# Performance work log

Hardware: AMD Instinct MI355X
Metric: run time of the kernel (lower is better)

The kernel has to match this reference:

```python
import jax, jax.numpy as jnp
import numpy as np

U, I, D, OUT = 8192, 16384, 64, 64

def setup_inputs() -> dict:
    key = jax.random.key(0)
    k1, k2, k3, k4 = jax.random.split(key, 4)
    user_emb = jax.random.normal(k1, (U, D), dtype=jnp.float32)
    item_emb = jax.random.normal(k2, (I, D), dtype=jnp.float32)
    attention_weight = jax.random.normal(k3, (D, OUT), dtype=jnp.float32) * (1.0 / np.sqrt(D))
    adj_matrix = jax.random.randint(k4, (U, I), 0, 2, dtype=jnp.int32)
    return {"user_emb": user_emb, "item_emb": item_emb,
            "attention_weight": attention_weight, "adj_matrix": adj_matrix}

def reference(user_emb, item_emb, attention_weight, adj_matrix):
    # score[u,i] = <user_emb[u], item_emb[i]>  (torch.inner)
    score = jnp.einsum('ud,id->ui', user_emb, item_emb)
    # mask non-edges to 0 (NOT -inf, faithful to torch.where(adj>0, score, 0))
    score = jnp.where(adj_matrix > 0, score, 0.0)
    score = jax.nn.softmax(score, axis=1)
    # flag == True path: aggregate items into users, then project
    output = score @ item_emb          # [U, D]
    output = output @ attention_weight  # [U, OUT]
    return output
```

## Files before the change

### kernel.cpp

```cpp
#include <hip/hip_runtime.h>
#include <hip/hip_bf16.h>
#include <math.h>

#define U_N   8192
#define I_N   16384
#define D_N   64
#define OUT_N 64
#define BN    32
#define NCH   8
#define ITERS 64
#define VN_ST 72
#define VT_ST 40
#define PL_ST 40

typedef _Float16 half8  __attribute__((ext_vector_type(8)));
typedef short    bf16x8 __attribute__((ext_vector_type(8)));
typedef short    bf16x4 __attribute__((ext_vector_type(4)));
typedef float    f32x4  __attribute__((ext_vector_type(4)));
typedef int      int4v  __attribute__((ext_vector_type(4)));

static __device__ __forceinline__ unsigned short f2bf(float f) {
    union { __hip_bfloat16 h; unsigned short u; } cv;
    cv.h = __float2bfloat16(f);
    return cv.u;
}
static __device__ __forceinline__ void bar() {
    asm volatile("s_waitcnt lgkmcnt(0)\n\ts_barrier" ::: "memory");
}

__global__ __launch_bounds__(256)
void prep_items(const float* __restrict__ item,
                _Float16* __restrict__ itemH,
                unsigned short* __restrict__ itemTt)
{
    const int i = blockIdx.x * 256 + threadIdx.x;
    const float* src = item + (size_t)i * D_N;
    f32x4 v[16];
    #pragma unroll
    for (int j = 0; j < 16; ++j) v[j] = *(const f32x4*)(src + 4 * j);

    #pragma unroll
    for (int j = 0; j < 8; ++j) {
        half8 h;
        #pragma unroll
        for (int k = 0; k < 4; ++k) { h[k] = (_Float16)v[2*j][k]; h[4+k] = (_Float16)v[2*j+1][k]; }
        *(half8*)&itemH[(size_t)i * D_N + 8 * j] = h;
    }
    const size_t tb = (size_t)(i >> 5) * (D_N * 32) + (i & 31);
    #pragma unroll
    for (int d = 0; d < 64; ++d)
        itemTt[tb + (size_t)d * 32] = f2bf(v[d >> 2][d & 3]);
}

#define DECL_SET(S) \
    int4v adj##S##a, adj##S##b; \
    half8 vn##S; bf16x8 vt##S;

#define LOAD_ADJ(S, tidx) do { \
    const size_t o_ = (size_t)(tidx) * BN; \
    adj##S##a = *(const int4v*)&adjq[o_];      \
    adj##S##b = *(const int4v*)&adjq[o_ + 16]; \
} while (0)

#define LOAD_TILE(S, tidx) do { \
    const size_t o_ = (size_t)(tidx) * BN; \
    vn##S = *(const half8*)&itemH[(ibase0 + o_ + (t >> 3)) * D_N + (t & 7) * 8]; \
    vt##S = *(const bf16x8*)&itemTt[((ibase0 + o_) >> 5) * (D_N * 32) \
                                    + (size_t)(t >> 2) * 32 + (t & 3) * 8]; \
} while (0)

#define COMMIT(S, bufw) do { \
    *(half8*)&Vn[bufw][(t >> 3) * VN_ST + (t & 7) * 8] = vn##S; \
    *(bf16x8*)&Vt[bufw][(t >> 2) * VT_ST + (t & 3) * 8] = vt##S; \
} while (0)

#define MASKS(S, ma, mb) \
    const unsigned ma = ((adj##S##a[0] != 0) ? 1u : 0u) | ((adj##S##a[1] != 0) ? 2u : 0u) | \
                        ((adj##S##a[2] != 0) ? 4u : 0u) | ((adj##S##a[3] != 0) ? 8u : 0u); \
    const unsigned mb = ((adj##S##b[0] != 0) ? 1u : 0u) | ((adj##S##b[1] != 0) ? 2u : 0u) | \
                        ((adj##S##b[2] != 0) ? 4u : 0u) | ((adj##S##b[3] != 0) ? 8u : 0u);

#define COMPUTE_REST(ma, mb, bufr) do { \
    half8 a00 = *(const half8*)&Vn[bufr][(c)      * VN_ST      + q * 8]; \
    half8 a01 = *(const half8*)&Vn[bufr][(c)      * VN_ST + 32 + q * 8]; \
    half8 a10 = *(const half8*)&Vn[bufr][(16 + c) * VN_ST      + q * 8]; \
    half8 a11 = *(const half8*)&Vn[bufr][(16 + c) * VN_ST + 32 + q * 8]; \
    bf16x8 v0 = *(const bf16x8*)&Vt[bufr][(c)      * VT_ST + q * 8]; \
    bf16x8 v1 = *(const bf16x8*)&Vt[bufr][(16 + c) * VT_ST + q * 8]; \
    bf16x8 v2 = *(const bf16x8*)&Vt[bufr][(32 + c) * VT_ST + q * 8]; \
    bf16x8 v3 = *(const bf16x8*)&Vt[bufr][(48 + c) * VT_ST + q * 8]; \
    f32x4 T0 = (f32x4){0.f,0.f,0.f,0.f}; \
    f32x4 T1 = (f32x4){0.f,0.f,0.f,0.f}; \
    T0 = __builtin_amdgcn_mfma_f32_16x16x32_f16(a00, ufrag0, T0, 0, 0, 0); \
    T0 = __builtin_amdgcn_mfma_f32_16x16x32_f16(a01, ufrag1, T0, 0, 0, 0); \
    T1 = __builtin_amdgcn_mfma_f32_16x16x32_f16(a10, ufrag0, T1, 0, 0, 0); \
    T1 = __builtin_amdgcn_mfma_f32_16x16x32_f16(a11, ufrag1, T1, 0, 0, 0); \
    bf16x4 p0, p1; \
    float e_; \
    e_ = __expf(((ma) & 1u) ? T0[0] : 0.0f); p0[0] = (short)f2bf(e_); lc += e_; \
    e_ = __expf(((ma) & 2u) ? T0[1] : 0.0f); p0[1] = (short)f2bf(e_); lc += e_; \
    e_ = __expf(((ma) & 4u) ? T0[2] : 0.0f); p0[2] = (short)f2bf(e_); lc += e_; \
    e_ = __expf(((ma) & 8u) ? T0[3] : 0.0f); p0[3] = (short)f2bf(e_); lc += e_; \
    e_ = __expf(((mb) & 1u) ? T1[0] : 0.0f); p1[0] = (short)f2bf(e_); lc += e_; \
    e_ = __expf(((mb) & 2u) ? T1[1] : 0.0f); p1[1] = (short)f2bf(e_); lc += e_; \
    e_ = __expf(((mb) & 4u) ? T1[2] : 0.0f); p1[2] = (short)f2bf(e_); lc += e_; \
    e_ = __expf(((mb) & 8u) ? T1[3] : 0.0f); p1[3] = (short)f2bf(e_); lc += e_; \
    *(bf16x4*)&plw[c * PL_ST + 4 * q]      = p0; \
    *(bf16x4*)&plw[c * PL_ST + 16 + 4 * q] = p1; \
    bf16x8 pf = *(const bf16x8*)&plw[c * PL_ST + q * 8]; \
    O0 = __builtin_amdgcn_mfma_f32_16x16x32_bf16(pf, v0, O0, 0, 0, 0); \
    O1 = __builtin_amdgcn_mfma_f32_16x16x32_bf16(pf, v1, O1, 0, 0, 0); \
    O2 = __builtin_amdgcn_mfma_f32_16x16x32_bf16(pf, v2, O2, 0, 0, 0); \
    O3 = __builtin_amdgcn_mfma_f32_16x16x32_bf16(pf, v3, O3, 0, 0, 0); \
} while (0)

__global__ __launch_bounds__(256, 3)
void atten_main(const float* __restrict__ user_emb,
                const _Float16* __restrict__ itemH,
                const unsigned short* __restrict__ itemTt,
                const int*   __restrict__ adj,
                float* __restrict__ wsO,
                float* __restrict__ wsL)
{
    __shared__ _Float16 Vn[2][BN * VN_ST];
    __shared__ short    Vt[2][D_N * VT_ST];
    __shared__ unsigned short Pl[4][16 * PL_ST];

    const int ch   = blockIdx.x;
    const int ub   = blockIdx.y;
    const int t    = threadIdx.x;
    const int w    = t >> 6;
    const int lane = t & 63;
    const int c    = lane & 15;
    const int q    = lane >> 4;

    const int    urow0  = ub * 64 + w * 16;
    const size_t ibase0 = (size_t)ch * (I_N / NCH);

    unsigned short* plw = &Pl[w][0];

    half8 ufrag0, ufrag1;
    {
        const float* up = user_emb + (size_t)(urow0 + c) * D_N + q * 8;
        f32x4 a0 = *(const f32x4*)(up);
        f32x4 b0 = *(const f32x4*)(up + 4);
        f32x4 a1 = *(const f32x4*)(up + 32);
        f32x4 b1 = *(const f32x4*)(up + 36);
        #pragma unroll
        for (int j = 0; j < 4; ++j) {
            ufrag0[j] = (_Float16)a0[j]; ufrag0[4 + j] = (_Float16)b0[j];
            ufrag1[j] = (_Float16)a1[j]; ufrag1[4 + j] = (_Float16)b1[j];
        }
    }

    f32x4 O0 = (f32x4){0.f,0.f,0.f,0.f};
    f32x4 O1 = O0, O2 = O0, O3 = O0;
    float lc = 0.f;

    const int* adjq = adj + (size_t)(urow0 + c) * I_N + ibase0 + 4 * q;

    DECL_SET(A)
    DECL_SET(B)

    LOAD_TILE(A, 0); LOAD_ADJ(A, 0);
    LOAD_TILE(B, 1); LOAD_ADJ(B, 1);
    COMMIT(A, 0);
    LOAD_TILE(A, 2);
    bar();

    for (int k = 0; k < ITERS; k += 2) {
        {
            MASKS(A, ma, mb)
            COMMIT(B, 1);
            const int ia = (k + 2 < ITERS) ? k + 2 : ITERS - 1;
            const int iv = (k + 3 < ITERS) ? k + 3 : ITERS - 1;
            LOAD_ADJ(A, ia);
            LOAD_TILE(B, iv);
            COMPUTE_REST(ma, mb, 0);
            bar();
        }
        {
            MASKS(B, ma, mb)
            COMMIT(A, 0);
            const int ia = (k + 3 < ITERS) ? k + 3 : ITERS - 1;
            const int iv = (k + 4 < ITERS) ? k + 4 : ITERS - 1;
            LOAD_ADJ(B, ia);
            LOAD_TILE(A, iv);
            COMPUTE_REST(ma, mb, 1);
            bar();
        }
    }

    lc += __shfl_xor(lc, 16);
    lc += __shfl_xor(lc, 32);

    {
        float* d0 = wsO + ((size_t)ch * U_N + urow0 + 4 * q + 0) * D_N;
        float* d1 = wsO + ((size_t)ch * U_N + urow0 + 4 * q + 1) * D_N;
        float* d2 = wsO + ((size_t)ch * U_N + urow0 + 4 * q + 2) * D_N;
        float* d3 = wsO + ((size_t)ch * U_N + urow0 + 4 * q + 3) * D_N;
        d0[c] = O0[0]; d0[16 + c] = O1[0]; d0[32 + c] = O2[0]; d0[48 + c] = O3[0];
        d1[c] = O0[1]; d1[16 + c] = O1[1]; d1[32 + c] = O2[1]; d1[48 + c] = O3[1];
        d2[c] = O0[2]; d2[16 + c] = O1[2]; d2[32 + c] = O2[2]; d2[48 + c] = O3[2];
        d3[c] = O0[3]; d3[16 + c] = O1[3]; d3[32 + c] = O2[3]; d3[48 + c] = O3[3];
    }
    if (q == 0)
        wsL[(size_t)ch * U_N + urow0 + c] = lc;
}

__global__ __launch_bounds__(256)
void atten_combine(const float* __restrict__ wsO,
                   const float* __restrict__ wsL,
                   const float* __restrict__ attw,
                   float* __restrict__ out,
                   int nch)
{
    __shared__ float inv[64];
    __shared__ float agg[64][68];
    __shared__ float Wl[64][68];

    const int t  = threadIdx.x;
    const int u0 = blockIdx.x * 64;

    {
        const int d = t >> 2, o0 = (t & 3) * 16;
        const float* src = attw + d * OUT_N + o0;
        #pragma unroll
        for (int j = 0; j < 4; ++j)
            *(f32x4*)&Wl[d][o0 + 4 * j] = *(const f32x4*)(src + 4 * j);
    }
    if (t < 64) {
        float L = 0.f;
        for (int cc = 0; cc < nch; ++cc) L += wsL[(size_t)cc * U_N + u0 + t];
        inv[t] = 1.0f / L;
    }
    __syncthreads();

    {
        const int ul = t >> 2, d0 = (t & 3) * 16;
        const int u = u0 + ul;
        f32x4 a4[4];
        #pragma unroll
        for (int j = 0; j < 4; ++j) a4[j] = (f32x4){0.f, 0.f, 0.f, 0.f};
        for (int cc = 0; cc < nch; ++cc) {
            const float* src = wsO + ((size_t)cc * U_N + u) * D_N + d0;
            #pragma unroll
            for (int j = 0; j < 4; ++j) a4[j] += *(const f32x4*)(src + 4 * j);
        }
        const float s = inv[ul];
        #pragma unroll
        for (int j = 0; j < 4; ++j)
            *(f32x4*)&agg[ul][d0 + 4 * j] = a4[j] * s;
    }
    __syncthreads();

    {
        const int ul = t >> 2, o0 = (t & 3) * 16;
        f32x4 acc[4];
        #pragma unroll
        for (int j = 0; j < 4; ++j) acc[j] = (f32x4){0.f, 0.f, 0.f, 0.f};
        for (int d = 0; d < 64; ++d) {
            const float av = agg[ul][d];
            #pragma unroll
            for (int j = 0; j < 4; ++j) {
                f32x4 wv = *(const f32x4*)&Wl[d][o0 + 4 * j];
                acc[j] += wv * av;
            }
        }
        float* dst = out + (size_t)(u0 + ul) * OUT_N + o0;
        #pragma unroll
        for (int j = 0; j < 4; ++j)
            *(f32x4*)(dst + 4 * j) = acc[j];
    }
}

extern "C" void kernel_launch(void* const* d_in, const int* in_sizes, int n_in,
                              void* d_out, int out_size, void* d_ws, size_t ws_size,
                              hipStream_t stream)
{
    const float* user_emb = (const float*)d_in[0];
    const float* item_emb = (const float*)d_in[1];
    const float* attw     = (const float*)d_in[2];
    const int*   adj      = (const int*)d_in[3];
    float* out = (float*)d_out;

    float*          wsO    = (float*)d_ws;
    float*          wsL    = wsO + (size_t)NCH * U_N * D_N;
    _Float16*       itemH  = (_Float16*)(wsL + (size_t)NCH * U_N);
    unsigned short* itemTt = (unsigned short*)(itemH + (size_t)I_N * D_N);

    prep_items<<<dim3(I_N / 256), 256, 0, stream>>>(item_emb, itemH, itemTt);
    atten_main<<<dim3(NCH, U_N / 64), 256, 0, stream>>>(user_emb, itemH, itemTt, adj,
                                                        wsO, wsL);
    atten_combine<<<dim3(U_N / 64), 256, 0, stream>>>(wsO, wsL, attw, out, NCH);
}
```

Before: 713.9 us.

## Pre-pack adjacency matrix into bitmasks before attention kernel

Adds a pack_adj kernel that reads the int32 adjacency matrix once and writes a bitmask in a layout tiled for the main kernel. The attention kernel then loads a few 32-bit mask words per tile instead of int4 adjacency vectors, which shrinks its memory traffic and register pressure and changes its prefetch schedule. The full 512MB adjacency read still happens in the packing kernel, so overall traffic falls only modestly, and the change adds a kernel launch and a mask write and read.

```diff
diff --git a/kernel.cpp b/kernel.cpp
--- a/kernel.cpp
+++ b/kernel.cpp
@@ -18,6 +18,7 @@
 typedef short    bf16x4 __attribute__((ext_vector_type(4)));
 typedef float    f32x4  __attribute__((ext_vector_type(4)));
 typedef int      int4v  __attribute__((ext_vector_type(4)));
+typedef unsigned uint4v __attribute__((ext_vector_type(4)));
 
 static __device__ __forceinline__ unsigned short f2bf(float f) {
     union { __hip_bfloat16 h; unsigned short u; } cv;
@@ -26,6 +27,30 @@
 }
 static __device__ __forceinline__ void bar() {
     asm volatile("s_waitcnt lgkmcnt(0)\n\ts_barrier" ::: "memory");
+}
+
+__global__ __launch_bounds__(256)
+void pack_adj(const int* __restrict__ adj, unsigned* __restrict__ mask)
+{
+    const int tid = blockIdx.x * 256 + threadIdx.x;
+    const int u   = tid >> 7;
+    const int w4  = tid & 127;
+    const int* src = adj + (size_t)u * I_N + w4 * 128;
+    uint4v mw;
+    #pragma unroll
+    for (int j = 0; j < 4; ++j) {
+        unsigned m = 0;
+        #pragma unroll
+        for (int i = 0; i < 8; ++i) {
+            int4v v = *(const int4v*)(src + j * 32 + i * 4);
+            m |= (v[0] != 0 ? (1u << (4 * i)) : 0u)
+               | (v[1] != 0 ? (2u << (4 * i)) : 0u)
+               | (v[2] != 0 ? (4u << (4 * i)) : 0u)
+               | (v[3] != 0 ? (8u << (4 * i)) : 0u);
+        }
+        mw[j] = m;
+    }
+    *(uint4v*)&mask[((((size_t)u >> 6) * 128 + w4) * 64 + (u & 63)) * 4] = mw;
 }
 
 __global__ __launch_bounds__(256)
@@ -52,15 +77,7 @@
         itemTt[tb + (size_t)d * 32] = f2bf(v[d >> 2][d & 3]);
 }
 
-#define DECL_SET(S) \
-    int4v adj##S##a, adj##S##b; \
-    half8 vn##S; bf16x8 vt##S;
-
-#define LOAD_ADJ(S, tidx) do { \
-    const size_t o_ = (size_t)(tidx) * BN; \
-    adj##S##a = *(const int4v*)&adjq[o_];      \
-    adj##S##b = *(const int4v*)&adjq[o_ + 16]; \
-} while (0)
+#define DECL_SET(S) half8 vn##S; bf16x8 vt##S;
 
 #define LOAD_TILE(S, tidx) do { \
     const size_t o_ = (size_t)(tidx) * BN; \
@@ -74,13 +91,7 @@
     *(bf16x8*)&Vt[bufw][(t >> 2) * VT_ST + (t & 3) * 8] = vt##S; \
 } while (0)
 
-#define MASKS(S, ma, mb) \
-    const unsigned ma = ((adj##S##a[0] != 0) ? 1u : 0u) | ((adj##S##a[1] != 0) ? 2u : 0u) | \
-                        ((adj##S##a[2] != 0) ? 4u : 0u) | ((adj##S##a[3] != 0) ? 8u : 0u); \
-    const unsigned mb = ((adj##S##b[0] != 0) ? 1u : 0u) | ((adj##S##b[1] != 0) ? 2u : 0u) | \
-                        ((adj##S##b[2] != 0) ? 4u : 0u) | ((adj##S##b[3] != 0) ? 8u : 0u);
-
-#define COMPUTE_REST(ma, mb, bufr) do { \
+#define COMPUTE_REST(mw, bufr) do { \
     half8 a00 = *(const half8*)&Vn[bufr][(c)      * VN_ST      + q * 8]; \
     half8 a01 = *(const half8*)&Vn[bufr][(c)      * VN_ST + 32 + q * 8]; \
     half8 a10 = *(const half8*)&Vn[bufr][(16 + c) * VN_ST      + q * 8]; \
@@ -95,16 +106,17 @@
     T0 = __builtin_amdgcn_mfma_f32_16x16x32_f16(a01, ufrag1, T0, 0, 0, 0); \
     T1 = __builtin_amdgcn_mfma_f32_16x16x32_f16(a10, ufrag0, T1, 0, 0, 0); \
     T1 = __builtin_amdgcn_mfma_f32_16x16x32_f16(a11, ufrag1, T1, 0, 0, 0); \
+    const unsigned ta_ = (mw) >> (4 * q); \
     bf16x4 p0, p1; \
     float e_; \
-    e_ = __expf(((ma) & 1u) ? T0[0] : 0.0f); p0[0] = (short)f2bf(e_); lc += e_; \
-    e_ = __expf(((ma) & 2u) ? T0[1] : 0.0f); p0[1] = (short)f2bf(e_); lc += e_; \
-    e_ = __expf(((ma) & 4u) ? T0[2] : 0.0f); p0[2] = (short)f2bf(e_); lc += e_; \
-    e_ = __expf(((ma) & 8u) ? T0[3] : 0.0f); p0[3] = (short)f2bf(e_); lc += e_; \
-    e_ = __expf(((mb) & 1u) ? T1[0] : 0.0f); p1[0] = (short)f2bf(e_); lc += e_; \
-    e_ = __expf(((mb) & 2u) ? T1[1] : 0.0f); p1[1] = (short)f2bf(e_); lc += e_; \
-    e_ = __expf(((mb) & 4u) ? T1[2] : 0.0f); p1[2] = (short)f2bf(e_); lc += e_; \
-    e_ = __expf(((mb) & 8u) ? T1[3] : 0.0f); p1[3] = (short)f2bf(e_); lc += e_; \
+    e_ = __expf((ta_ & 0x1u)     ? T0[0] : 0.0f); p0[0] = (short)f2bf(e_); lc += e_; \
+    e_ = __expf((ta_ & 0x2u)     ? T0[1] : 0.0f); p0[1] = (short)f2bf(e_); lc += e_; \
+    e_ = __expf((ta_ & 0x4u)     ? T0[2] : 0.0f); p0[2] = (short)f2bf(e_); lc += e_; \
+    e_ = __expf((ta_ & 0x8u)     ? T0[3] : 0.0f); p0[3] = (short)f2bf(e_); lc += e_; \
+    e_ = __expf((ta_ & 0x10000u) ? T1[0] : 0.0f); p1[0] = (short)f2bf(e_); lc += e_; \
+    e_ = __expf((ta_ & 0x20000u) ? T1[1] : 0.0f); p1[1] = (short)f2bf(e_); lc += e_; \
+    e_ = __expf((ta_ & 0x40000u) ? T1[2] : 0.0f); p1[2] = (short)f2bf(e_); lc += e_; \
+    e_ = __expf((ta_ & 0x80000u) ? T1[3] : 0.0f); p1[3] = (short)f2bf(e_); lc += e_; \
     *(bf16x4*)&plw[c * PL_ST + 4 * q]      = p0; \
     *(bf16x4*)&plw[c * PL_ST + 16 + 4 * q] = p1; \
     bf16x8 pf = *(const bf16x8*)&plw[c * PL_ST + q * 8]; \
@@ -114,11 +126,22 @@
     O3 = __builtin_amdgcn_mfma_f32_16x16x32_bf16(pf, v3, O3, 0, 0, 0); \
 } while (0)
 
+#define PAIR(k, m0, m1) do { \
+    COMMIT(B, 1); \
+    LOAD_TILE(B, ((k) + 3 < ITERS) ? (k) + 3 : ITERS - 1); \
+    COMPUTE_REST(m0, 0); \
+    bar(); \
+    COMMIT(A, 0); \
+    LOAD_TILE(A, ((k) + 4 < ITERS) ? (k) + 4 : ITERS - 1); \
+    COMPUTE_REST(m1, 1); \
+    bar(); \
+} while (0)
+
 __global__ __launch_bounds__(256, 3)
 void atten_main(const float* __restrict__ user_emb,
                 const _Float16* __restrict__ itemH,
                 const unsigned short* __restrict__ itemTt,
-                const int*   __restrict__ adj,
+                const unsigned* __restrict__ mask,
                 float* __restrict__ wsO,
                 float* __restrict__ wsL)
 {
@@ -136,8 +159,11 @@
 
     const int    urow0  = ub * 64 + w * 16;
     const size_t ibase0 = (size_t)ch * (I_N / NCH);
+    const int    uu     = w * 16 + c;
 
     unsigned short* plw = &Pl[w][0];
+
+    const unsigned* mb = mask + ((size_t)(ub * 128 + ch * 16) * 64 + uu) * 4;
 
     half8 ufrag0, ufrag1;
     {
@@ -157,38 +183,26 @@
     f32x4 O1 = O0, O2 = O0, O3 = O0;
     float lc = 0.f;
 
-    const int* adjq = adj + (size_t)(urow0 + c) * I_N + ibase0 + 4 * q;
-
     DECL_SET(A)
     DECL_SET(B)
-
-    LOAD_TILE(A, 0); LOAD_ADJ(A, 0);
-    LOAD_TILE(B, 1); LOAD_ADJ(B, 1);
+    uint4v Mx, My;
+
+    LOAD_TILE(A, 0);
+    LOAD_TILE(B, 1);
+    Mx = *(const uint4v*)&mb[0];
+    My = *(const uint4v*)&mb[256];
     COMMIT(A, 0);
     LOAD_TILE(A, 2);
     bar();
 
-    for (int k = 0; k < ITERS; k += 2) {
-        {
-            MASKS(A, ma, mb)
-            COMMIT(B, 1);
-            const int ia = (k + 2 < ITERS) ? k + 2 : ITERS - 1;
-            const int iv = (k + 3 < ITERS) ? k + 3 : ITERS - 1;
-            LOAD_ADJ(A, ia);
-            LOAD_TILE(B, iv);
-            COMPUTE_REST(ma, mb, 0);
-            bar();
-        }
-        {
-            MASKS(B, ma, mb)
-            COMMIT(A, 0);
-            const int ia = (k + 3 < ITERS) ? k + 3 : ITERS - 1;
-            const int iv = (k + 4 < ITERS) ? k + 4 : ITERS - 1;
-            LOAD_ADJ(B, ia);
-            LOAD_TILE(A, iv);
-            COMPUTE_REST(ma, mb, 1);
-            bar();
-        }
+    for (int hb = 0; hb < 16; hb += 2) {
+        const int k0 = hb * 4;
+        PAIR(k0,     Mx[0], Mx[1]);
+        PAIR(k0 + 2, Mx[2], Mx[3]);
+        Mx = *(const uint4v*)&mb[(size_t)((hb + 2 < 16) ? hb + 2 : 15) * 256];
+        PAIR(k0 + 4, My[0], My[1]);
+        PAIR(k0 + 6, My[2], My[3]);
+        My = *(const uint4v*)&mb[(size_t)((hb + 3 < 16) ? hb + 3 : 15) * 256];
     }
 
     lc += __shfl_xor(lc, 16);
@@ -288,9 +302,11 @@
     float*          wsL    = wsO + (size_t)NCH * U_N * D_N;
     _Float16*       itemH  = (_Float16*)(wsL + (size_t)NCH * U_N);
     unsigned short* itemTt = (unsigned short*)(itemH + (size_t)I_N * D_N);
-
+    unsigned*       mask   = (unsigned*)(itemTt + (size_t)I_N * D_N);
+
+    pack_adj<<<dim3(U_N * 128 / 256), 256, 0, stream>>>(adj, mask);
     prep_items<<<dim3(I_N / 256), 256, 0, stream>>>(item_emb, itemH, itemTt);
-    atten_main<<<dim3(NCH, U_N / 64), 256, 0, stream>>>(user_emb, itemH, itemTt, adj,
+    atten_main<<<dim3(NCH, U_N / 64), 256, 0, stream>>>(user_emb, itemH, itemTt, mask,
                                                         wsO, wsL);
     atten_combine<<<dim3(U_N / 64), 256, 0, stream>>>(wsO, wsL, attw, out, NCH);
 }
```

Result: slower. 793.6 us (+11.2%).

## Feed softmax probabilities straight into 16x16x16 bf16 MFMA, dropping LDS round-trip

Applied to the files above, without the earlier changes.

The P·V product now uses the K=16 bf16 MFMA so the exp results already in registers can serve directly as the A operand. This removes the per-wave LDS staging buffer for probabilities (a write, a read and its latency). It costs twice as many smaller MFMAs and more LDS reads for V fragments. The item dimension is also split into 16 chunks instead of 8, and the occupancy hint is raised from 3 to 4 blocks per CU.

```diff
diff --git a/kernel.cpp b/kernel.cpp
--- a/kernel.cpp
+++ b/kernel.cpp
@@ -7,11 +7,10 @@
 #define D_N   64
 #define OUT_N 64
 #define BN    32
-#define NCH   8
-#define ITERS 64
+#define NCH   16
+#define ITERS 32
 #define VN_ST 72
 #define VT_ST 40
-#define PL_ST 40
 
 typedef _Float16 half8  __attribute__((ext_vector_type(8)));
 typedef short    bf16x8 __attribute__((ext_vector_type(8)));
@@ -26,6 +25,16 @@
 }
 static __device__ __forceinline__ void bar() {
     asm volatile("s_waitcnt lgkmcnt(0)\n\ts_barrier" ::: "memory");
+}
+static __device__ __forceinline__ f32x4 pv_mfma(bf16x4 a, bf16x4 b, f32x4 c) {
+#if __has_builtin(__builtin_amdgcn_mfma_f32_16x16x16bf16_1k)
+    return __builtin_amdgcn_mfma_f32_16x16x16bf16_1k(a, b, c, 0, 0, 0);
+#else
+    f32x4 d;
+    asm volatile("v_mfma_f32_16x16x16_bf16 %0, %1, %2, %3"
+                 : "=v"(d) : "v"(a), "v"(b), "v"(c));
+    return d;
+#endif
 }
 
 __global__ __launch_bounds__(256)
@@ -85,10 +94,6 @@
     half8 a01 = *(const half8*)&Vn[bufr][(c)      * VN_ST + 32 + q * 8]; \
     half8 a10 = *(const half8*)&Vn[bufr][(16 + c) * VN_ST      + q * 8]; \
     half8 a11 = *(const half8*)&Vn[bufr][(16 + c) * VN_ST + 32 + q * 8]; \
-    bf16x8 v0 = *(const bf16x8*)&Vt[bufr][(c)      * VT_ST + q * 8]; \
-    bf16x8 v1 = *(const bf16x8*)&Vt[bufr][(16 + c) * VT_ST + q * 8]; \
-    bf16x8 v2 = *(const bf16x8*)&Vt[bufr][(32 + c) * VT_ST + q * 8]; \
-    bf16x8 v3 = *(const bf16x8*)&Vt[bufr][(48 + c) * VT_ST + q * 8]; \
     f32x4 T0 = (f32x4){0.f,0.f,0.f,0.f}; \
     f32x4 T1 = (f32x4){0.f,0.f,0.f,0.f}; \
     T0 = __builtin_amdgcn_mfma_f32_16x16x32_f16(a00, ufrag0, T0, 0, 0, 0); \
@@ -105,16 +110,21 @@
     e_ = __expf(((mb) & 2u) ? T1[1] : 0.0f); p1[1] = (short)f2bf(e_); lc += e_; \
     e_ = __expf(((mb) & 4u) ? T1[2] : 0.0f); p1[2] = (short)f2bf(e_); lc += e_; \
     e_ = __expf(((mb) & 8u) ? T1[3] : 0.0f); p1[3] = (short)f2bf(e_); lc += e_; \
-    *(bf16x4*)&plw[c * PL_ST + 4 * q]      = p0; \
-    *(bf16x4*)&plw[c * PL_ST + 16 + 4 * q] = p1; \
-    bf16x8 pf = *(const bf16x8*)&plw[c * PL_ST + q * 8]; \
-    O0 = __builtin_amdgcn_mfma_f32_16x16x32_bf16(pf, v0, O0, 0, 0, 0); \
-    O1 = __builtin_amdgcn_mfma_f32_16x16x32_bf16(pf, v1, O1, 0, 0, 0); \
-    O2 = __builtin_amdgcn_mfma_f32_16x16x32_bf16(pf, v2, O2, 0, 0, 0); \
-    O3 = __builtin_amdgcn_mfma_f32_16x16x32_bf16(pf, v3, O3, 0, 0, 0); \
+    bf16x4 vb00 = *(const bf16x4*)&Vt[bufr][(c)      * VT_ST      + 4 * q]; \
+    bf16x4 vb01 = *(const bf16x4*)&Vt[bufr][(c)      * VT_ST + 16 + 4 * q]; \
+    bf16x4 vb10 = *(const bf16x4*)&Vt[bufr][(16 + c) * VT_ST      + 4 * q]; \
+    bf16x4 vb11 = *(const bf16x4*)&Vt[bufr][(16 + c) * VT_ST + 16 + 4 * q]; \
+    bf16x4 vb20 = *(const bf16x4*)&Vt[bufr][(32 + c) * VT_ST      + 4 * q]; \
+    bf16x4 vb21 = *(const bf16x4*)&Vt[bufr][(32 + c) * VT_ST + 16 + 4 * q]; \
+    bf16x4 vb30 = *(const bf16x4*)&Vt[bufr][(48 + c) * VT_ST      + 4 * q]; \
+    bf16x4 vb31 = *(const bf16x4*)&Vt[bufr][(48 + c) * VT_ST + 16 + 4 * q]; \
+    O0 = pv_mfma(p0, vb00, O0);  O0 = pv_mfma(p1, vb01, O0); \
+    O1 = pv_mfma(p0, vb10, O1);  O1 = pv_mfma(p1, vb11, O1); \
+    O2 = pv_mfma(p0, vb20, O2);  O2 = pv_mfma(p1, vb21, O2); \
+    O3 = pv_mfma(p0, vb30, O3);  O3 = pv_mfma(p1, vb31, O3); \
 } while (0)
 
-__global__ __launch_bounds__(256, 3)
+__global__ __launch_bounds__(256, 4)
 void atten_main(const float* __restrict__ user_emb,
                 const _Float16* __restrict__ itemH,
                 const unsigned short* __restrict__ itemTt,
@@ -124,7 +134,6 @@
 {
     __shared__ _Float16 Vn[2][BN * VN_ST];
     __shared__ short    Vt[2][D_N * VT_ST];
-    __shared__ unsigned short Pl[4][16 * PL_ST];
 
     const int ch   = blockIdx.x;
     const int ub   = blockIdx.y;
@@ -136,8 +145,6 @@
 
     const int    urow0  = ub * 64 + w * 16;
     const size_t ibase0 = (size_t)ch * (I_N / NCH);
-
-    unsigned short* plw = &Pl[w][0];
 
     half8 ufrag0, ufrag1;
     {
```

Result: slower. 740.7 us (+3.8%).
